# Kernel optimization log

Measured on AMD Instinct MI355X. Metric: run time of the kernel, lower is better.

The kernel has to match this reference:

```python
import jax, jax.numpy as jnp
import numpy as np

INF = 1.0e6
SIGMA = 1.0
RADIUS = 2.5
M, N, H, K, C_IN, C_OUT = 50000, 50000, 32, 15, 128, 128
EXTENT = 10.0  # spatial extent of the random point cloud


def setup_inputs() -> dict:
    key = jax.random.key(0)
    k1, k2, k3, k4, k5, k6 = jax.random.split(key, 6)
    q_pts = jax.random.uniform(k1, (M, 3), dtype=jnp.float32) * EXTENT
    s_pts = jax.random.uniform(k2, (N, 3), dtype=jnp.float32) * EXTENT
    s_feats = jax.random.normal(k3, (N, C_IN), dtype=jnp.float32)
    neighb_inds = jax.random.randint(k4, (M, H), 0, N, dtype=jnp.int64)
    # kernel points: random points inside sphere of given radius (stand-in for load_kernels)
    kp = jax.random.normal(k5, (K, 3), dtype=jnp.float32)
    kp = kp / jnp.linalg.norm(kp, axis=1, keepdims=True) * (RADIUS * 0.66)
    kernel_points = kp.at[0].set(0.0)  # fixed center point
    # kaiming-uniform-like init
    bound = 1.0 / np.sqrt(C_IN)
    weights = jax.random.uniform(k6, (K, C_IN, C_OUT), dtype=jnp.float32,
                                 minval=-bound, maxval=bound)
    return {"q_pts": q_pts, "s_pts": s_pts, "s_feats": s_feats,
            "neighb_inds": neighb_inds, "kernel_points": kernel_points,
            "weights": weights}


def reference(q_pts, s_pts, s_feats, neighb_inds, kernel_points, weights):
    # pad support points with a far-away point so out-of-range indices get zero influence
    s_pts_pad = jnp.concatenate([s_pts, jnp.full((1, 3), INF, s_pts.dtype)], axis=0)
    neighbors = s_pts_pad[neighb_inds] - q_pts[:, None, :]          # (M, H, 3)
    diffs = neighbors[:, :, None, :] - kernel_points[None, None]    # (M, H, K, 3)
    sq_dist = jnp.sum(diffs * diffs, axis=-1)                       # (M, H, K)
    # linear influence, clipped at 0 (no_grad in torch -> stop_gradient here)
    w = jnp.clip(1.0 - jnp.sqrt(sq_dist) / SIGMA, 0.0)              # (M, H, K)
    neighbor_weights = jax.lax.stop_gradient(jnp.swapaxes(w, 1, 2)) # (M, K, H)
    # gather neighbor features (padded with a zero row)
    feats_pad = jnp.concatenate([s_feats, jnp.zeros((1, s_feats.shape[1]), s_feats.dtype)], axis=0)
    neighbor_feats = feats_pad[neighb_inds]                         # (M, H, C_in)
    weighted_feats = jnp.matmul(neighbor_weights, neighbor_feats)   # (M, K, C_in)
    return jnp.einsum('mkc,kcd->md', weighted_feats, weights)       # (M, C_out)
```

## Files before the change

### kernel.cpp

```cpp
#include <hip/hip_runtime.h>

#define M_Q 50000
#define N_S 50000
#define H_N 32
#define K_P 15
#define C_IN 128
#define C_OUT 128
#define QB 64
#define NT 512
#define EMAX 24

typedef __attribute__((ext_vector_type(8))) short s8v;
typedef __attribute__((ext_vector_type(4))) float f4v;
typedef __attribute__((ext_vector_type(4))) float fl4;
typedef __attribute__((ext_vector_type(4))) unsigned u4v;

union AF { u4v u; s8v s; };

static __device__ __forceinline__ unsigned f2bf_bits(float x) {
    union { float f; unsigned u; } v; v.f = x;
    return (v.u + 0x7fffu + ((v.u >> 16) & 1u)) >> 16;
}
static __device__ __forceinline__ unsigned pack_bf16(float a, float b) {
    return f2bf_bits(a) | (f2bf_bits(b) << 16);
}

__global__ __launch_bounds__(256) void wcvt_frag(const float* __restrict__ W,
                                                 unsigned short* __restrict__ Wtf) {
    int i = blockIdx.x * 256 + threadIdx.x;
    if (i >= K_P * 2 * 4 * 4 * 64) return;
    const int lane = i & 63;
    int r = i >> 6;
    const int kk = r & 3; r >>= 2;
    const int ct = r & 3; r >>= 2;
    const int cw = r & 1;
    const int k  = r >> 1;
    const int d  = cw * 64 + ct * 16 + (lane & 15);
    const int c0 = kk * 32 + (lane >> 4) * 8;
    unsigned short* dst = Wtf + (size_t)i * 8;
    #pragma unroll
    for (int j = 0; j < 8; ++j)
        dst[j] = (unsigned short)f2bf_bits(W[((size_t)k * 128 + c0 + j) * 128 + d]);
}

template <typename IT>
__global__ __launch_bounds__(NT, 4) void kpconv_v6(
    const float* __restrict__ q_pts,
    const float* __restrict__ s_pts,
    const float* __restrict__ s_feats,
    const IT* __restrict__ inds,
    const float* __restrict__ kernel_points,
    const unsigned short* __restrict__ Wtf,
    float* __restrict__ out)
{
    __shared__ unsigned short s_B[2 * 4 * 4 * 64 * 8];
    __shared__ float s_ew[QB][EMAX];
    __shared__ unsigned s_em[QB][EMAX];
    __shared__ int s_cnt[QB];
    __shared__ float s_kp[K_P * 3];
    __shared__ float s_q[QB * 3];

    const int t = threadIdx.x;
    const int lane = t & 63;
    const int w = t >> 6;
    const int quad = lane >> 4, l15 = lane & 15;
    const int qbase = blockIdx.x * QB;

    if (t < K_P * 3) s_kp[t] = kernel_points[t];
    if (t < QB) s_cnt[t] = 0;
    if (t < QB * 3) {
        int g = qbase * 3 + t;
        s_q[t] = (g < M_Q * 3) ? q_pts[g] : 0.0f;
    }
    __syncthreads();

    #pragma unroll
    for (int it = 0; it < 4; ++it) {
        const int task = it * NT + t;
        const int q = task >> 5, h = task & 31;
        const int qg = qbase + q;
        if (qg < M_Q) {
            long long idx = (long long)inds[(size_t)qg * H_N + h];
            if ((unsigned long long)idx < (unsigned long long)N_S) {
                const int i32 = (int)idx;
                const float rx = s_pts[i32 * 3 + 0] - s_q[q * 3 + 0];
                const float ry = s_pts[i32 * 3 + 1] - s_q[q * 3 + 1];
                const float rz = s_pts[i32 * 3 + 2] - s_q[q * 3 + 2];
                #pragma unroll
                for (int k = 0; k < K_P; ++k) {
                    const float dx = rx - s_kp[k * 3 + 0];
                    const float dy = ry - s_kp[k * 3 + 1];
                    const float dz = rz - s_kp[k * 3 + 2];
                    const float d2 = dx * dx + dy * dy + dz * dz;
                    if (d2 < 1.0f) {
                        const float wgt = 1.0f - sqrtf(d2);
                        const int pos = atomicAdd(&s_cnt[q], 1);
                        if (pos < EMAX) {
                            s_ew[q][pos] = wgt;
                            s_em[q][pos] = ((unsigned)k << 16) | (unsigned)i32;
                        }
                    }
                }
            }
        }
    }
    __syncthreads();

    if (t < QB) {
        const int n = min(s_cnt[t], EMAX);
        s_cnt[t] = n;
        for (int i = 1; i < n; ++i) {
            const unsigned mi = s_em[t][i];
            const float wi = s_ew[t][i];
            int j = i - 1;
            while (j >= 0 && s_em[t][j] > mi) {
                s_em[t][j + 1] = s_em[t][j];
                s_ew[t][j + 1] = s_ew[t][j];
                --j;
            }
            s_em[t][j + 1] = mi;
            s_ew[t][j + 1] = wi;
        }
    }
    __syncthreads();

    const int q = (w & 3) * 16 + l15;
    const int cw = w >> 2;
    const int cnt = s_cnt[q];
    int ptr = 0;
    unsigned meta = (cnt > 0) ? s_em[q][0] : 0xffffffffu;

    const f4v zf = {0.0f, 0.0f, 0.0f, 0.0f};
    f4v acc[4]; acc[0] = zf; acc[1] = zf; acc[2] = zf; acc[3] = zf;
    float va[4][8];
    #pragma unroll
    for (int kk = 0; kk < 4; ++kk)
        #pragma unroll
        for (int j = 0; j < 8; ++j) va[kk][j] = 0.0f;
    AF af[4];
    #pragma unroll
    for (int kk = 0; kk < 4; ++kk) af[kk].u = (u4v){0u, 0u, 0u, 0u};

    for (int k = 0; k < K_P; ++k) {
        const u4v* bsrc = ((const u4v*)Wtf) + (size_t)k * 2048 + t;
        const u4v b0 = bsrc[0], b1 = bsrc[512], b2 = bsrc[1024], b3 = bsrc[1536];

        bool built = false;
        while (true) {
            const bool m = ((int)(meta >> 16) == k);
            if (!__any(m)) break;
            if (m) {
                const float wgt = s_ew[q][ptr];
                const float* fr = s_feats + (size_t)(meta & 0xffffu) * C_IN + quad * 8;
                #pragma unroll
                for (int kk = 0; kk < 4; ++kk) {
                    const fl4 f0 = *(const fl4*)(fr + kk * 32);
                    const fl4 f1 = *(const fl4*)(fr + kk * 32 + 4);
                    va[kk][0] = fmaf(wgt, f0.x, va[kk][0]);
                    va[kk][1] = fmaf(wgt, f0.y, va[kk][1]);
                    va[kk][2] = fmaf(wgt, f0.z, va[kk][2]);
                    va[kk][3] = fmaf(wgt, f0.w, va[kk][3]);
                    va[kk][4] = fmaf(wgt, f1.x, va[kk][4]);
                    va[kk][5] = fmaf(wgt, f1.y, va[kk][5]);
                    va[kk][6] = fmaf(wgt, f1.z, va[kk][6]);
                    va[kk][7] = fmaf(wgt, f1.w, va[kk][7]);
                }
                built = true;
                ++ptr;
                meta = (ptr < cnt) ? s_em[q][ptr] : 0xffffffffu;
            }
        }
        const unsigned long long anyb = __ballot(built);
        if (built) {
            #pragma unroll
            for (int kk = 0; kk < 4; ++kk) {
                af[kk].u[0] = pack_bf16(va[kk][0], va[kk][1]);
                af[kk].u[1] = pack_bf16(va[kk][2], va[kk][3]);
                af[kk].u[2] = pack_bf16(va[kk][4], va[kk][5]);
                af[kk].u[3] = pack_bf16(va[kk][6], va[kk][7]);
                #pragma unroll
                for (int j = 0; j < 8; ++j) va[kk][j] = 0.0f;
            }
        }

        {
            u4v* bdst = ((u4v*)s_B) + t;
            bdst[0] = b0; bdst[512] = b1; bdst[1024] = b2; bdst[1536] = b3;
        }
        __syncthreads();

        if (anyb) {
            #pragma unroll
            for (int ct = 0; ct < 4; ++ct) {
                #pragma unroll
                for (int kk = 0; kk < 4; ++kk) {
                    const int slot = ((cw * 4 + ct) * 4 + kk) * 64 + lane;
                    const s8v b = *(const s8v*)(s_B + (size_t)slot * 8);
                    acc[ct] = __builtin_amdgcn_mfma_f32_16x16x32_bf16(af[kk].s, b, acc[ct], 0, 0, 0);
                }
            }
        }
        if (built) {
            #pragma unroll
            for (int kk = 0; kk < 4; ++kk) af[kk].u = (u4v){0u, 0u, 0u, 0u};
        }
        __syncthreads();
    }

    #pragma unroll
    for (int ct = 0; ct < 4; ++ct) {
        #pragma unroll
        for (int r = 0; r < 4; ++r) {
            const int qg = qbase + (w & 3) * 16 + quad * 4 + r;
            if (qg < M_Q)
                out[(size_t)qg * C_OUT + cw * 64 + ct * 16 + l15] = acc[ct][r];
        }
    }
}

extern "C" void kernel_launch(void* const* d_in, const int* in_sizes, int n_in,
                              void* d_out, int out_size, void* d_ws, size_t ws_size,
                              hipStream_t stream) {
    const float* q_pts         = (const float*)d_in[0];
    const float* s_pts         = (const float*)d_in[1];
    const float* s_feats       = (const float*)d_in[2];
    const float* kernel_points = (const float*)d_in[4];
    const float* weights       = (const float*)d_in[5];
    float* out = (float*)d_out;
    const bool i64 = (in_sizes[3] == 2 * M_Q * H_N);

    unsigned short* Wtf = (unsigned short*)d_ws;
    const int slots = K_P * 2 * 4 * 4 * 64;
    wcvt_frag<<<(slots + 255) / 256, 256, 0, stream>>>(weights, Wtf);

    dim3 grid((M_Q + QB - 1) / QB), block(NT);
    if (i64)
        kpconv_v6<long long><<<grid, block, 0, stream>>>(
            q_pts, s_pts, s_feats, (const long long*)d_in[3], kernel_points, Wtf, out);
    else
        kpconv_v6<int><<<grid, block, 0, stream>>>(
            q_pts, s_pts, s_feats, (const int*)d_in[3], kernel_points, Wtf, out);
}
```

Before: 183.9 us.

## Drop shared-memory weight staging; each wave owns all query rows and two column tiles

Halves the block to 256 threads. Each wave now handles all 64 queries (4 row tiles) against its own 32 output columns and loads B fragments straight from global into registers, so the LDS weight buffer and the two per-kernel-point __syncthreads are gone. The weight fragment layout changes to match. The cost is redundant gathering: every wave rebuilds the A fragments for all 64 queries (4x the feature gathers per block), register pressure goes up (launch bounds change to 3), and the divergent gather loops are now serialized per row tile.

```diff
diff --git a/kernel.cpp b/kernel.cpp
--- a/kernel.cpp
+++ b/kernel.cpp
@@ -7,7 +7,7 @@
 #define C_IN 128
 #define C_OUT 128
 #define QB 64
-#define NT 512
+#define NT 256
 #define EMAX 24
 
 typedef __attribute__((ext_vector_type(8))) short s8v;
@@ -28,14 +28,12 @@
 __global__ __launch_bounds__(256) void wcvt_frag(const float* __restrict__ W,
                                                  unsigned short* __restrict__ Wtf) {
     int i = blockIdx.x * 256 + threadIdx.x;
-    if (i >= K_P * 2 * 4 * 4 * 64) return;
+    if (i >= K_P * 8 * 4 * 64) return;
     const int lane = i & 63;
-    int r = i >> 6;
-    const int kk = r & 3; r >>= 2;
-    const int ct = r & 3; r >>= 2;
-    const int cw = r & 1;
-    const int k  = r >> 1;
-    const int d  = cw * 64 + ct * 16 + (lane & 15);
+    const int kk = (i >> 6) & 3;
+    const int col = (i >> 8) & 7;
+    const int k = i >> 11;
+    const int d = col * 16 + (lane & 15);
     const int c0 = kk * 32 + (lane >> 4) * 8;
     unsigned short* dst = Wtf + (size_t)i * 8;
     #pragma unroll
@@ -44,7 +42,7 @@
 }
 
 template <typename IT>
-__global__ __launch_bounds__(NT, 4) void kpconv_v6(
+__global__ __launch_bounds__(NT, 3) void kpconv_v7(
     const float* __restrict__ q_pts,
     const float* __restrict__ s_pts,
     const float* __restrict__ s_feats,
@@ -53,7 +51,6 @@
     const unsigned short* __restrict__ Wtf,
     float* __restrict__ out)
 {
-    __shared__ unsigned short s_B[2 * 4 * 4 * 64 * 8];
     __shared__ float s_ew[QB][EMAX];
     __shared__ unsigned s_em[QB][EMAX];
     __shared__ int s_cnt[QB];
@@ -75,7 +72,7 @@
     __syncthreads();
 
     #pragma unroll
-    for (int it = 0; it < 4; ++it) {
+    for (int it = 0; it < 8; ++it) {
         const int task = it * NT + t;
         const int q = task >> 5, h = task & 31;
         const int qg = qbase + q;
@@ -124,96 +121,102 @@
     }
     __syncthreads();
 
-    const int q = (w & 3) * 16 + l15;
-    const int cw = w >> 2;
-    const int cnt = s_cnt[q];
-    int ptr = 0;
-    unsigned meta = (cnt > 0) ? s_em[q][0] : 0xffffffffu;
+    int ptr[4], ecnt[4];
+    unsigned meta[4];
+    #pragma unroll
+    for (int mt = 0; mt < 4; ++mt) {
+        const int q = mt * 16 + l15;
+        ecnt[mt] = s_cnt[q];
+        ptr[mt] = 0;
+        meta[mt] = (ecnt[mt] > 0) ? s_em[q][0] : 0xffffffffu;
+    }
 
     const f4v zf = {0.0f, 0.0f, 0.0f, 0.0f};
-    f4v acc[4]; acc[0] = zf; acc[1] = zf; acc[2] = zf; acc[3] = zf;
+    f4v acc[4][2];
+    #pragma unroll
+    for (int mt = 0; mt < 4; ++mt) { acc[mt][0] = zf; acc[mt][1] = zf; }
+
     float va[4][8];
     #pragma unroll
     for (int kk = 0; kk < 4; ++kk)
         #pragma unroll
         for (int j = 0; j < 8; ++j) va[kk][j] = 0.0f;
-    AF af[4];
-    #pragma unroll
-    for (int kk = 0; kk < 4; ++kk) af[kk].u = (u4v){0u, 0u, 0u, 0u};
 
     for (int k = 0; k < K_P; ++k) {
-        const u4v* bsrc = ((const u4v*)Wtf) + (size_t)k * 2048 + t;
-        const u4v b0 = bsrc[0], b1 = bsrc[512], b2 = bsrc[1024], b3 = bsrc[1536];
-
-        bool built = false;
-        while (true) {
-            const bool m = ((int)(meta >> 16) == k);
-            if (!__any(m)) break;
-            if (m) {
-                const float wgt = s_ew[q][ptr];
-                const float* fr = s_feats + (size_t)(meta & 0xffffu) * C_IN + quad * 8;
+        u4v b[2][4];
+        #pragma unroll
+        for (int nc = 0; nc < 2; ++nc) {
+            const int c8 = w * 2 + nc;
+            const u4v* bsrc = ((const u4v*)Wtf) + ((((size_t)k * 8 + c8) * 4) * 64 + lane);
+            #pragma unroll
+            for (int kk = 0; kk < 4; ++kk) b[nc][kk] = bsrc[kk * 64];
+        }
+
+        #pragma unroll
+        for (int mt = 0; mt < 4; ++mt) {
+            const int q = mt * 16 + l15;
+            bool built = false;
+            while (true) {
+                const bool m = ((int)(meta[mt] >> 16) == k);
+                if (!__any(m)) break;
+                if (m) {
+                    const float wgt = s_ew[q][ptr[mt]];
+                    const float* fr = s_feats + (size_t)(meta[mt] & 0xffffu) * C_IN + quad * 8;
+                    #pragma unroll
+                    for (int kk = 0; kk < 4; ++kk) {
+                        const fl4 f0 = *(const fl4*)(fr + kk * 32);
+                        const fl4 f1 = *(const fl4*)(fr + kk * 32 + 4);
+                        va[kk][0] = fmaf(wgt, f0.x, va[kk][0]);
+                        va[kk][1] = fmaf(wgt, f0.y, va[kk][1]);
+                        va[kk][2] = fmaf(wgt, f0.z, va[kk][2]);
+                        va[kk][3] = fmaf(wgt, f0.w, va[kk][3]);
+                        va[kk][4] = fmaf(wgt, f1.x, va[kk][4]);
+                        va[kk][5] = fmaf(wgt, f1.y, va[kk][5]);
+                        va[kk][6] = fmaf(wgt, f1.z, va[kk][6]);
+                        va[kk][7] = fmaf(wgt, f1.w, va[kk][7]);
+                    }
+                    built = true;
+                    ++ptr[mt];
+                    meta[mt] = (ptr[mt] < ecnt[mt]) ? s_em[q][ptr[mt]] : 0xffffffffu;
+                }
+            }
+            const unsigned long long anyb = __ballot(built);
+            if (anyb) {
+                AF af[4];
+                if (built) {
+                    #pragma unroll
+                    for (int kk = 0; kk < 4; ++kk) {
+                        af[kk].u[0] = pack_bf16(va[kk][0], va[kk][1]);
+                        af[kk].u[1] = pack_bf16(va[kk][2], va[kk][3]);
+                        af[kk].u[2] = pack_bf16(va[kk][4], va[kk][5]);
+                        af[kk].u[3] = pack_bf16(va[kk][6], va[kk][7]);
+                        #pragma unroll
+                        for (int j = 0; j < 8; ++j) va[kk][j] = 0.0f;
+                    }
+                } else {
+                    #pragma unroll
+                    for (int kk = 0; kk < 4; ++kk) af[kk].u = (u4v){0u, 0u, 0u, 0u};
+                }
                 #pragma unroll
-                for (int kk = 0; kk < 4; ++kk) {
-                    const fl4 f0 = *(const fl4*)(fr + kk * 32);
-                    const fl4 f1 = *(const fl4*)(fr + kk * 32 + 4);
-                    va[kk][0] = fmaf(wgt, f0.x, va[kk][0]);
-                    va[kk][1] = fmaf(wgt, f0.y, va[kk][1]);
-                    va[kk][2] = fmaf(wgt, f0.z, va[kk][2]);
-                    va[kk][3] = fmaf(wgt, f0.w, va[kk][3]);
-                    va[kk][4] = fmaf(wgt, f1.x, va[kk][4]);
-                    va[kk][5] = fmaf(wgt, f1.y, va[kk][5]);
-                    va[kk][6] = fmaf(wgt, f1.z, va[kk][6]);
-                    va[kk][7] = fmaf(wgt, f1.w, va[kk][7]);
-                }
-                built = true;
-                ++ptr;
-                meta = (ptr < cnt) ? s_em[q][ptr] : 0xffffffffu;
-            }
-        }
-        const unsigned long long anyb = __ballot(built);
-        if (built) {
+                for (int nc = 0; nc < 2; ++nc)
+                    #pragma unroll
+                    for (int kk = 0; kk < 4; ++kk)
+                        acc[mt][nc] = __builtin_amdgcn_mfma_f32_16x16x32_bf16(
+                            af[kk].s, *(const s8v*)&b[nc][kk], acc[mt][nc], 0, 0, 0);
+            }
+        }
+    }
+
+    #pragma unroll
+    for (int mt = 0; mt < 4; ++mt) {
+        #pragma unroll
+        for (int nc = 0; nc < 2; ++nc) {
             #pragma unroll
-            for (int kk = 0; kk < 4; ++kk) {
-                af[kk].u[0] = pack_bf16(va[kk][0], va[kk][1]);
-                af[kk].u[1] = pack_bf16(va[kk][2], va[kk][3]);
-                af[kk].u[2] = pack_bf16(va[kk][4], va[kk][5]);
-                af[kk].u[3] = pack_bf16(va[kk][6], va[kk][7]);
-                #pragma unroll
-                for (int j = 0; j < 8; ++j) va[kk][j] = 0.0f;
-            }
-        }
-
-        {
-            u4v* bdst = ((u4v*)s_B) + t;
-            bdst[0] = b0; bdst[512] = b1; bdst[1024] = b2; bdst[1536] = b3;
-        }
-        __syncthreads();
-
-        if (anyb) {
-            #pragma unroll
-            for (int ct = 0; ct < 4; ++ct) {
-                #pragma unroll
-                for (int kk = 0; kk < 4; ++kk) {
-                    const int slot = ((cw * 4 + ct) * 4 + kk) * 64 + lane;
-                    const s8v b = *(const s8v*)(s_B + (size_t)slot * 8);
-                    acc[ct] = __builtin_amdgcn_mfma_f32_16x16x32_bf16(af[kk].s, b, acc[ct], 0, 0, 0);
-                }
-            }
-        }
-        if (built) {
-            #pragma unroll
-            for (int kk = 0; kk < 4; ++kk) af[kk].u = (u4v){0u, 0u, 0u, 0u};
-        }
-        __syncthreads();
-    }
-
-    #pragma unroll
-    for (int ct = 0; ct < 4; ++ct) {
-        #pragma unroll
-        for (int r = 0; r < 4; ++r) {
-            const int qg = qbase + (w & 3) * 16 + quad * 4 + r;
-            if (qg < M_Q)
-                out[(size_t)qg * C_OUT + cw * 64 + ct * 16 + l15] = acc[ct][r];
+            for (int r = 0; r < 4; ++r) {
+                const int qg = qbase + mt * 16 + quad * 4 + r;
+                if (qg < M_Q)
+                    out[(size_t)qg * C_OUT + (w * 2 + nc) * 16 + l15] = acc[mt][nc][r];
+            }
         }
     }
 }
@@ -230,14 +233,14 @@
     const bool i64 = (in_sizes[3] == 2 * M_Q * H_N);
 
     unsigned short* Wtf = (unsigned short*)d_ws;
-    const int slots = K_P * 2 * 4 * 4 * 64;
+    const int slots = K_P * 8 * 4 * 64;
     wcvt_frag<<<(slots + 255) / 256, 256, 0, stream>>>(weights, Wtf);
 
     dim3 grid((M_Q + QB - 1) / QB), block(NT);
     if (i64)
-        kpconv_v6<long long><<<grid, block, 0, stream>>>(
+        kpconv_v7<long long><<<grid, block, 0, stream>>>(
             q_pts, s_pts, s_feats, (const long long*)d_in[3], kernel_points, Wtf, out);
     else
-        kpconv_v6<int><<<grid, block, 0, stream>>>(
+        kpconv_v7<int><<<grid, block, 0, stream>>>(
             q_pts, s_pts, s_feats, (const int*)d_in[3], kernel_points, Wtf, out);
 }
```

Measured after the change: 221.0 us. +20.1%, slower.
